# Kernel optimization log

Hardware: AMD Instinct MI355X
Metric: run time of the kernel (lower is better)

The kernel has to match this reference:

```python
import jax, jax.numpy as jnp
import numpy as np

N = 50000   # nodes
E = 800000  # edges
IN = 128    # input feature dim
HID = 64    # hidden per head
HEADS = 2
P = 100000  # pos/neg pairs
SLOPE = 0.2 # DGL GATConv default negative_slope
EPS = 1e-5  # BatchNorm eps


def setup_inputs() -> dict:
    key = jax.random.key(0)
    ks = jax.random.split(key, 40)
    nrm = lambda k, s, sc=0.1: jax.random.normal(k, s, jnp.float32) * sc
    inp = {}
    inp['x'] = jax.random.normal(ks[0], (N, IN), jnp.float32)
    inp['edge_src'] = jax.random.randint(ks[1], (E,), 0, N)
    inp['edge_dst'] = jax.random.randint(ks[2], (E,), 0, N)
    inp['pos_src'] = jax.random.randint(ks[3], (P,), 0, N)
    inp['pos_dst'] = jax.random.randint(ks[4], (P,), 0, N)
    inp['neg_src'] = jax.random.randint(ks[5], (P,), 0, N)
    inp['neg_dst'] = jax.random.randint(ks[6], (P,), 0, N)
    # GATConv layer 0: in=IN, out=HID, heads=HEADS
    inp['W0'] = nrm(ks[7], (IN, HEADS * HID))
    inp['al0'] = nrm(ks[8], (HEADS, HID))
    inp['ar0'] = nrm(ks[9], (HEADS, HID))
    inp['b0'] = jnp.zeros((HEADS * HID,), jnp.float32)
    # GATConv layer 1: in=HEADS*HID, out=HID, heads=HEADS
    inp['W1'] = nrm(ks[10], (HEADS * HID, HEADS * HID))
    inp['al1'] = nrm(ks[11], (HEADS, HID))
    inp['ar1'] = nrm(ks[12], (HEADS, HID))
    inp['b1'] = jnp.zeros((HEADS * HID,), jnp.float32)
    # GATConv layer 2: in=HEADS*HID, out=HID, heads=1
    inp['W2'] = nrm(ks[13], (HEADS * HID, HID))
    inp['al2'] = nrm(ks[14], (1, HID))
    inp['ar2'] = nrm(ks[15], (1, HID))
    inp['b2'] = jnp.zeros((HID,), jnp.float32)
    # BatchNorm params
    inp['bn0_g'] = jnp.ones((HEADS * HID,), jnp.float32)
    inp['bn0_b'] = jnp.zeros((HEADS * HID,), jnp.float32)
    inp['bn1_g'] = jnp.ones((HEADS * HID,), jnp.float32)
    inp['bn1_b'] = jnp.zeros((HEADS * HID,), jnp.float32)
    # predictor MLP: HID->HID->HID->1
    inp['pW1'] = nrm(ks[16], (HID, HID))
    inp['pb1'] = jnp.zeros((HID,), jnp.float32)
    inp['pW2'] = nrm(ks[17], (HID, HID))
    inp['pb2'] = jnp.zeros((HID,), jnp.float32)
    inp['pW3'] = nrm(ks[18], (HID, 1))
    inp['pb3'] = jnp.zeros((1,), jnp.float32)
    return inp


def gat_conv(h, src, dst, W, al, ar, b, heads, fh):
    # DGL GATConv: fc -> per-node attn dots -> edge LeakyReLU -> dst-segment softmax -> scatter-add
    feat = (h @ W).reshape(-1, heads, fh)            # [N, H, F]
    el = (feat * al[None]).sum(-1)                   # [N, H]
    er = (feat * ar[None]).sum(-1)                   # [N, H]
    e = jax.nn.leaky_relu(el[src] + er[dst], SLOPE)  # [E, H]
    m = jax.ops.segment_max(e, dst, num_segments=N)  # per-dst max for stability
    ee = jnp.exp(e - m[dst])
    denom = jax.ops.segment_sum(ee, dst, num_segments=N)
    alpha = ee / jnp.maximum(denom[dst], 1e-9)       # [E, H]
    out = jax.ops.segment_sum(alpha[:, :, None] * feat[src], dst, num_segments=N)
    return (out + b.reshape(1, heads, fh)).reshape(-1, heads * fh)


def batch_norm(h, g, b):
    mu = h.mean(0)
    var = jnp.var(h, 0)  # biased, matches torch BN training normalization
    return g * (h - mu) * jax.lax.rsqrt(var + EPS) + b


def predict(h_src, h_dst, pW1, pb1, pW2, pb2, pW3, pb3):
    z = h_src * h_dst
    z = jax.nn.relu(z @ pW1 + pb1)
    z = jax.nn.relu(z @ pW2 + pb2)
    return z @ pW3 + pb3


def reference(x, edge_src, edge_dst, pos_src, pos_dst, neg_src, neg_dst,
              W0, al0, ar0, b0, W1, al1, ar1, b1, W2, al2, ar2, b2,
              bn0_g, bn0_b, bn1_g, bn1_b, pW1, pb1, pW2, pb2, pW3, pb3):
    h = gat_conv(x, edge_src, edge_dst, W0, al0, ar0, b0, HEADS, HID)
    h = jax.nn.relu(batch_norm(h, bn0_g, bn0_b))  # dropout = identity (eval)
    h = gat_conv(h, edge_src, edge_dst, W1, al1, ar1, b1, HEADS, HID)
    h = jax.nn.relu(batch_norm(h, bn1_g, bn1_b))
    h = gat_conv(h, edge_src, edge_dst, W2, al2, ar2, b2, 1, HID)  # [N, HID]
    h_pos = predict(h[pos_src], h[pos_dst], pW1, pb1, pW2, pb2, pW3, pb3)
    h_neg = predict(h[neg_src], h[neg_dst], pW1, pb1, pW2, pb2, pW3, pb3)
    return (h_pos, h_neg)
```

## Files before the change

### kernel.cpp

```cpp
#include <hip/hip_runtime.h>
#include <hip/hip_fp16.h>
#include <cstdint>
#include <cstddef>

#define N_NODES 50000
#define N_EDGES 800000

typedef _Float16 f16x8 __attribute__((ext_vector_type(8)));
typedef float f32x4 __attribute__((ext_vector_type(4)));

__global__ void f32_to_f16(const float* __restrict__ in, __half* __restrict__ outp, int n4)
{
    int i = blockIdx.x * blockDim.x + threadIdx.x;
    int stride = gridDim.x * blockDim.x;
    for (; i < n4; i += stride) {
        float4 v = *reinterpret_cast<const float4*>(in + (size_t)i * 4);
        __half2 a = __floats2half2_rn(v.x, v.y);
        __half2 b = __floats2half2_rn(v.z, v.w);
        uint2 pk;
        pk.x = *reinterpret_cast<unsigned*>(&a);
        pk.y = *reinterpret_cast<unsigned*>(&b);
        *reinterpret_cast<uint2*>(outp + (size_t)i * 4) = pk;
    }
}

__global__ void prep_wt(const float* __restrict__ W0, const float* __restrict__ W1,
                        const float* __restrict__ W2, __half* __restrict__ t0,
                        __half* __restrict__ t1, __half* __restrict__ t2)
{
    int b = blockIdx.x >> 7;
    int k = blockIdx.x & 127;
    int c = threadIdx.x;
    const float* W = (b == 0) ? W0 : (b == 1) ? W1 : W2;
    __half* T = (b == 0) ? t0 : (b == 1) ? t1 : t2;
    int Cb = (b == 2) ? 64 : 128;
    if (c < Cb) T[(size_t)c * 128 + k] = __float2half(W[(size_t)k * Cb + c]);
}

template <int C, int H>
__launch_bounds__(256, 3)
__global__ void gemm_mfma(const __half* __restrict__ Ah, const __half* __restrict__ Wt,
                          const float* __restrict__ al, const float* __restrict__ ar,
                          __half* __restrict__ feat, float* __restrict__ el,
                          float* __restrict__ er, int n)
{
    constexpr int K = 128;
    constexpr int AS = 136;
    constexpr int CT = C / 16;
    __shared__ __half As[64 * AS];
    __shared__ __half Ws[C * AS];

    const int tid = threadIdx.x;
    const int brow = blockIdx.x * 64;

    for (int idx = tid; idx < 64 * 16; idx += 256) {
        int r = idx >> 4, u = idx & 15;
        int gr = brow + r;
        f16x8 v = {0, 0, 0, 0, 0, 0, 0, 0};
        if (gr < n) v = *reinterpret_cast<const f16x8*>(Ah + (size_t)gr * K + u * 8);
        *reinterpret_cast<f16x8*>(&As[r * AS + u * 8]) = v;
    }
    for (int idx = tid; idx < C * 16; idx += 256) {
        int c = idx >> 4, u = idx & 15;
        *reinterpret_cast<f16x8*>(&Ws[c * AS + u * 8]) =
            *reinterpret_cast<const f16x8*>(Wt + (size_t)c * K + u * 8);
    }
    __syncthreads();

    const int w = tid >> 6;
    const int l = tid & 63;
    const int l15 = l & 15;
    const int kg = l >> 4;

    f32x4 acc[CT];
    #pragma unroll
    for (int ct = 0; ct < CT; ++ct) acc[ct] = (f32x4){0.f, 0.f, 0.f, 0.f};

    #pragma unroll
    for (int kt = 0; kt < 4; ++kt) {
        f16x8 a = *reinterpret_cast<const f16x8*>(&As[(w * 16 + l15) * AS + kt * 32 + kg * 8]);
        #pragma unroll
        for (int ct = 0; ct < CT; ++ct) {
            f16x8 b = *reinterpret_cast<const f16x8*>(&Ws[(ct * 16 + l15) * AS + kt * 32 + kg * 8]);
            acc[ct] = __builtin_amdgcn_mfma_f32_16x16x32_f16(a, b, acc[ct], 0, 0, 0);
        }
    }

    const int row0 = w * 16 + kg * 4;
    float pel[4][H], per_[4][H];
    #pragma unroll
    for (int j = 0; j < 4; ++j)
        #pragma unroll
        for (int h = 0; h < H; ++h) { pel[j][h] = 0.f; per_[j][h] = 0.f; }

    #pragma unroll
    for (int ct = 0; ct < CT; ++ct) {
        int col = ct * 16 + l15;
        int head = (H == 2) ? (col >> 6) : 0;
        int lc = col & 63;
        float av = al[head * 64 + lc];
        float rv = ar[head * 64 + lc];
        #pragma unroll
        for (int j = 0; j < 4; ++j) {
            float fv = acc[ct][j];
            int gr = brow + row0 + j;
            if (gr < n) feat[(size_t)gr * C + col] = __float2half(fv);
            pel[j][head] += fv * av;
            per_[j][head] += fv * rv;
        }
    }
    #pragma unroll
    for (int off = 1; off < 16; off <<= 1) {
        #pragma unroll
        for (int j = 0; j < 4; ++j)
            #pragma unroll
            for (int h = 0; h < H; ++h) {
                pel[j][h] += __shfl_xor(pel[j][h], off, 64);
                per_[j][h] += __shfl_xor(per_[j][h], off, 64);
            }
    }
    if (l15 == 0) {
        #pragma unroll
        for (int j = 0; j < 4; ++j) {
            int gr = brow + row0 + j;
            if (gr < n) {
                if constexpr (H == 2) {
                    float2 e0 = make_float2(pel[j][0], pel[j][1]);
                    float2 e1 = make_float2(per_[j][0], per_[j][1]);
                    *reinterpret_cast<float2*>(el + (size_t)gr * 2) = e0;
                    *reinterpret_cast<float2*>(er + (size_t)gr * 2) = e1;
                } else {
                    el[gr] = pel[j][0];
                    er[gr] = per_[j][0];
                }
            }
        }
    }
}

__global__ void hist_dst(const int* __restrict__ dst, int* __restrict__ cnt, int E)
{
    int e = blockIdx.x * blockDim.x + threadIdx.x;
    if (e < E) atomicAdd(&cnt[dst[e]], 1);
}

__global__ void scan_block_sums(const int* __restrict__ cnt, int* __restrict__ bsum, int n)
{
    __shared__ int sh[256];
    int i = blockIdx.x * 256 + threadIdx.x;
    sh[threadIdx.x] = (i < n) ? cnt[i] : 0;
    __syncthreads();
    for (int off = 128; off; off >>= 1) {
        if (threadIdx.x < off) sh[threadIdx.x] += sh[threadIdx.x + off];
        __syncthreads();
    }
    if (threadIdx.x == 0) bsum[blockIdx.x] = sh[0];
}

__global__ void scan_bsum(int* __restrict__ bsum, int nb)
{
    __shared__ int sh[256];
    int t = threadIdx.x;
    sh[t] = (t < nb) ? bsum[t] : 0;
    __syncthreads();
    for (int off = 1; off < 256; off <<= 1) {
        int u = (t >= off) ? sh[t - off] : 0;
        __syncthreads();
        sh[t] += u;
        __syncthreads();
    }
    if (t < nb) bsum[t] = t ? sh[t - 1] : 0;
}

__global__ void scan_final(const int* __restrict__ cnt, const int* __restrict__ bsum,
                           int* __restrict__ rs, int* __restrict__ cursor, int n)
{
    __shared__ int sh[256];
    int t = threadIdx.x;
    int i = blockIdx.x * 256 + t;
    int v = (i < n) ? cnt[i] : 0;
    sh[t] = v;
    __syncthreads();
    for (int off = 1; off < 256; off <<= 1) {
        int u = (t >= off) ? sh[t - off] : 0;
        __syncthreads();
        sh[t] += u;
        __syncthreads();
    }
    int excl = sh[t] - v + bsum[blockIdx.x];
    if (i < n) { rs[i] = excl; cursor[i] = excl; }
    if (i == n - 1) rs[n] = excl + v;
}

__global__ void scatter_csr(const int* __restrict__ src, const int* __restrict__ dst,
                            int* __restrict__ cursor, int* __restrict__ csr, int E)
{
    int e = blockIdx.x * blockDim.x + threadIdx.x;
    if (e < E) {
        int d = dst[e];
        int pos = atomicAdd(&cursor[d], 1);
        csr[pos] = src[e];
    }
}

template <int C, int H>
__launch_bounds__(256)
__global__ void gat_agg(const int* __restrict__ rs, const int* __restrict__ csr,
                        const float* __restrict__ el, const float* __restrict__ er,
                        const __half* __restrict__ feat, const float* __restrict__ bias,
                        float* __restrict__ outp, int n)
{
    int node = blockIdx.x * 4 + (threadIdx.x >> 6);
    if (node >= n) return;
    int lane = threadIdx.x & 63;
    int start = rs[node], end = rs[node + 1];

    if constexpr (H == 2) {
        float2 e2 = *reinterpret_cast<const float2*>(er + (size_t)node * 2);
        float m0 = -INFINITY, m1 = -INFINITY;
        for (int j = start + lane; j < end; j += 64) {
            int s = csr[j];
            float2 l2 = *reinterpret_cast<const float2*>(el + (size_t)s * 2);
            float v0 = l2.x + e2.x; v0 = v0 >= 0.f ? v0 : 0.2f * v0;
            float v1 = l2.y + e2.y; v1 = v1 >= 0.f ? v1 : 0.2f * v1;
            m0 = fmaxf(m0, v0); m1 = fmaxf(m1, v1);
        }
        #pragma unroll
        for (int off = 32; off; off >>= 1) {
            m0 = fmaxf(m0, __shfl_xor(m0, off, 64));
            m1 = fmaxf(m1, __shfl_xor(m1, off, 64));
        }
        const int slot = lane >> 4;
        const int cl = lane & 15;
        const int h = cl >> 3;
        const float mh = h ? m1 : m0;
        const float erh = h ? e2.y : e2.x;
        float ssum = 0.f;
        float acc[8];
        #pragma unroll
        for (int u = 0; u < 8; ++u) acc[u] = 0.f;
        for (int j = start + slot; j < end; j += 4) {
            int s = csr[j];
            float v = el[(size_t)s * 2 + h] + erh;
            v = v >= 0.f ? v : 0.2f * v;
            float p = __expf(v - mh);
            ssum += p;
            float4 raw = *reinterpret_cast<const float4*>(feat + (size_t)s * C + cl * 8);
            const __half2* hp = reinterpret_cast<const __half2*>(&raw);
            #pragma unroll
            for (int u = 0; u < 4; ++u) {
                float2 f2 = __half22float2(hp[u]);
                acc[2 * u]     = fmaf(p, f2.x, acc[2 * u]);
                acc[2 * u + 1] = fmaf(p, f2.y, acc[2 * u + 1]);
            }
        }
        #pragma unroll
        for (int off = 16; off <= 32; off <<= 1) {
            ssum += __shfl_xor(ssum, off, 64);
            #pragma unroll
            for (int u = 0; u < 8; ++u) acc[u] += __shfl_xor(acc[u], off, 64);
        }
        if (slot == 0) {
            float r = 1.f / fmaxf(ssum, 1e-9f);
            float4 o0 = make_float4(acc[0] * r, acc[1] * r, acc[2] * r, acc[3] * r);
            float4 o1 = make_float4(acc[4] * r, acc[5] * r, acc[6] * r, acc[7] * r);
            *reinterpret_cast<float4*>(outp + (size_t)node * C + cl * 8) = o0;
            *reinterpret_cast<float4*>(outp + (size_t)node * C + cl * 8 + 4) = o1;
        }
    } else {
        float er0 = er[node];
        float m0 = -INFINITY;
        for (int j = start + lane; j < end; j += 64) {
            int s = csr[j];
            float v = el[s] + er0;
            v = v >= 0.f ? v : 0.2f * v;
            m0 = fmaxf(m0, v);
        }
        #pragma unroll
        for (int off = 32; off; off >>= 1)
            m0 = fmaxf(m0, __shfl_xor(m0, off, 64));
        const int slot = lane >> 3;
        const int cl = lane & 7;
        float ssum = 0.f;
        float acc[8];
        #pragma unroll
        for (int u = 0; u < 8; ++u) acc[u] = 0.f;
        for (int j = start + slot; j < end; j += 8) {
            int s = csr[j];
            float v = el[s] + er0;
            v = v >= 0.f ? v : 0.2f * v;
            float p = __expf(v - m0);
            ssum += p;
            float4 raw = *reinterpret_cast<const float4*>(feat + (size_t)s * C + cl * 8);
            const __half2* hp = reinterpret_cast<const __half2*>(&raw);
            #pragma unroll
            for (int u = 0; u < 4; ++u) {
                float2 f2 = __half22float2(hp[u]);
                acc[2 * u]     = fmaf(p, f2.x, acc[2 * u]);
                acc[2 * u + 1] = fmaf(p, f2.y, acc[2 * u + 1]);
            }
        }
        #pragma unroll
        for (int off = 8; off <= 32; off <<= 1) {
            ssum += __shfl_xor(ssum, off, 64);
            #pragma unroll
            for (int u = 0; u < 8; ++u) acc[u] += __shfl_xor(acc[u], off, 64);
        }
        if (slot == 0) {
            float r = 1.f / fmaxf(ssum, 1e-9f);
            float4 o0, o1;
            o0.x = acc[0] * r + bias[cl * 8 + 0];
            o0.y = acc[1] * r + bias[cl * 8 + 1];
            o0.z = acc[2] * r + bias[cl * 8 + 2];
            o0.w = acc[3] * r + bias[cl * 8 + 3];
            o1.x = acc[4] * r + bias[cl * 8 + 4];
            o1.y = acc[5] * r + bias[cl * 8 + 5];
            o1.z = acc[6] * r + bias[cl * 8 + 6];
            o1.w = acc[7] * r + bias[cl * 8 + 7];
            *reinterpret_cast<float4*>(outp + (size_t)node * C + cl * 8) = o0;
            *reinterpret_cast<float4*>(outp + (size_t)node * C + cl * 8 + 4) = o1;
        }
    }
}

__global__ void bn_stats(const float* __restrict__ h, float* __restrict__ sums, int n)
{
    __shared__ float s1[256], s2[256];
    int c = threadIdx.x & 127, half = threadIdx.x >> 7;
    float ls = 0.f, lq = 0.f;
    for (int r = blockIdx.x * 2 + half; r < n; r += gridDim.x * 2) {
        float v = h[(size_t)r * 128 + c];
        ls += v; lq += v * v;
    }
    s1[threadIdx.x] = ls; s2[threadIdx.x] = lq;
    __syncthreads();
    if (threadIdx.x < 128) {
        atomicAdd(&sums[c], s1[threadIdx.x] + s1[threadIdx.x + 128]);
        atomicAdd(&sums[128 + c], s2[threadIdx.x] + s2[threadIdx.x + 128]);
    }
}

__global__ void bn_apply(const float* __restrict__ in, __half* __restrict__ outp,
                         const float* __restrict__ sums,
                         const float* __restrict__ g, const float* __restrict__ b,
                         long long npairs)
{
    long long i = (long long)blockIdx.x * blockDim.x + threadIdx.x;
    if (i >= npairs) return;
    int c0 = (int)((i * 2) & 127);
    const float invN = 1.f / (float)N_NODES;
    float2 v = *reinterpret_cast<const float2*>(in + i * 2);
    float mean0 = sums[c0] * invN, mean1 = sums[c0 + 1] * invN;
    float var0 = sums[128 + c0] * invN - mean0 * mean0;
    float var1 = sums[128 + c0 + 1] * invN - mean1 * mean1;
    float o0 = fmaxf((v.x - mean0) * rsqrtf(var0 + 1e-5f) * g[c0] + b[c0], 0.f);
    float o1 = fmaxf((v.y - mean1) * rsqrtf(var1 + 1e-5f) * g[c0 + 1] + b[c0 + 1], 0.f);
    *reinterpret_cast<__half2*>(outp + i * 2) = __floats2half2_rn(o0, o1);
}

__launch_bounds__(256, 3)
__global__ void predictor(const float* __restrict__ h,
                          const int* __restrict__ ps, const int* __restrict__ pd,
                          const int* __restrict__ ns, const int* __restrict__ nd,
                          const float* __restrict__ W1, const float* __restrict__ b1,
                          const float* __restrict__ W2, const float* __restrict__ b2,
                          const float* __restrict__ W3, const float* __restrict__ b3,
                          float* __restrict__ out, int P)
{
    __shared__ float w1[64 * 64];
    __shared__ float w2[64 * 64];
    __shared__ float zt[64 * 68];
    const int tid = threadIdx.x;

    for (int i = tid; i < 1024; i += 256) {
        *reinterpret_cast<float4*>(&w1[i * 4]) = *reinterpret_cast<const float4*>(W1 + i * 4);
        *reinterpret_cast<float4*>(&w2[i * 4]) = *reinterpret_cast<const float4*>(W2 + i * 4);
    }

    {
        int l = tid & 63, w = tid >> 6;
        int gp = blockIdx.x * 64 + l;
        int s, d;
        if (gp < P) { s = ps[gp]; d = pd[gp]; }
        else        { s = ns[gp - P]; d = nd[gp - P]; }
        const float4* hs = reinterpret_cast<const float4*>(h + (size_t)s * 64 + w * 16);
        const float4* hd = reinterpret_cast<const float4*>(h + (size_t)d * 64 + w * 16);
        #pragma unroll
        for (int j = 0; j < 4; ++j) {
            float4 a = hs[j], b = hd[j];
            int c0 = w * 16 + j * 4;
            zt[(c0 + 0) * 68 + l] = a.x * b.x;
            zt[(c0 + 1) * 68 + l] = a.y * b.y;
            zt[(c0 + 2) * 68 + l] = a.z * b.z;
            zt[(c0 + 3) * 68 + l] = a.w * b.w;
        }
    }
    __syncthreads();

    const int pb = tid >> 4;
    const int cb = tid & 15;
    const int p0 = pb * 4, c0 = cb * 4;
    float4 vb1 = *reinterpret_cast<const float4*>(b1 + c0);
    float4 vb2 = *reinterpret_cast<const float4*>(b2 + c0);
    float4 vw3 = *reinterpret_cast<const float4*>(W3 + c0);
    const float b3v = b3[0];

    float acc[4][4];

    #pragma unroll
    for (int i = 0; i < 4; ++i)
        #pragma unroll
        for (int j = 0; j < 4; ++j) acc[i][j] = 0.f;

    #pragma unroll 4
    for (int k = 0; k < 64; ++k) {
        float4 zv = *reinterpret_cast<const float4*>(&zt[k * 68 + p0]);
        float4 wv = *reinterpret_cast<const float4*>(&w1[k * 64 + c0]);
        float zz[4] = {zv.x, zv.y, zv.z, zv.w};
        float ww[4] = {wv.x, wv.y, wv.z, wv.w};
        #pragma unroll
        for (int i = 0; i < 4; ++i)
            #pragma unroll
            for (int j = 0; j < 4; ++j)
                acc[i][j] = fmaf(zz[i], ww[j], acc[i][j]);
    }
    __syncthreads();
    {
        float bb[4] = {vb1.x, vb1.y, vb1.z, vb1.w};
        #pragma unroll
        for (int j = 0; j < 4; ++j) {
            float4 st = make_float4(fmaxf(acc[0][j] + bb[j], 0.f),
                                    fmaxf(acc[1][j] + bb[j], 0.f),
                                    fmaxf(acc[2][j] + bb[j], 0.f),
                                    fmaxf(acc[3][j] + bb[j], 0.f));
            *reinterpret_cast<float4*>(&zt[(c0 + j) * 68 + p0]) = st;
        }
    }
    __syncthreads();

    #pragma unroll
    for (int i = 0; i < 4; ++i)
        #pragma unroll
        for (int j = 0; j < 4; ++j) acc[i][j] = 0.f;

    #pragma unroll 4
    for (int k = 0; k < 64; ++k) {
        float4 zv = *reinterpret_cast<const float4*>(&zt[k * 68 + p0]);
        float4 wv = *reinterpret_cast<const float4*>(&w2[k * 64 + c0]);
        float zz[4] = {zv.x, zv.y, zv.z, zv.w};
        float ww[4] = {wv.x, wv.y, wv.z, wv.w};
        #pragma unroll
        for (int i = 0; i < 4; ++i)
            #pragma unroll
            for (int j = 0; j < 4; ++j)
                acc[i][j] = fmaf(zz[i], ww[j], acc[i][j]);
    }

    float part[4];
    {
        float bb[4] = {vb2.x, vb2.y, vb2.z, vb2.w};
        float w3v[4] = {vw3.x, vw3.y, vw3.z, vw3.w};
        #pragma unroll
        for (int i = 0; i < 4; ++i) {
            float su = 0.f;
            #pragma unroll
            for (int j = 0; j < 4; ++j)
                su += fmaxf(acc[i][j] + bb[j], 0.f) * w3v[j];
            part[i] = su;
        }
    }
    #pragma unroll
    for (int off = 1; off < 16; off <<= 1) {
        #pragma unroll
        for (int i = 0; i < 4; ++i)
            part[i] += __shfl_xor(part[i], off, 16);
    }
    if (cb == 0) {
        int gp0 = blockIdx.x * 64 + p0;
        #pragma unroll
        for (int i = 0; i < 4; ++i)
            out[gp0 + i] = part[i] + b3v;
    }
}

extern "C" void kernel_launch(void* const* d_in, const int* in_sizes, int n_in,
                              void* d_out, int out_size, void* d_ws, size_t ws_size,
                              hipStream_t stream)
{
    const float* x    = (const float*)d_in[0];
    const int* es     = (const int*)d_in[1];
    const int* ed     = (const int*)d_in[2];
    const int* ps     = (const int*)d_in[3];
    const int* pdst   = (const int*)d_in[4];
    const int* ns     = (const int*)d_in[5];
    const int* nd     = (const int*)d_in[6];
    const float* W0   = (const float*)d_in[7];
    const float* al0  = (const float*)d_in[8];
    const float* ar0  = (const float*)d_in[9];
    const float* W1   = (const float*)d_in[11];
    const float* al1  = (const float*)d_in[12];
    const float* ar1  = (const float*)d_in[13];
    const float* W2   = (const float*)d_in[15];
    const float* al2  = (const float*)d_in[16];
    const float* ar2  = (const float*)d_in[17];
    const float* b2   = (const float*)d_in[18];
    const float* bn0g = (const float*)d_in[19];
    const float* bn0b = (const float*)d_in[20];
    const float* bn1g = (const float*)d_in[21];
    const float* bn1b = (const float*)d_in[22];
    const float* pW1  = (const float*)d_in[23];
    const float* pb1  = (const float*)d_in[24];
    const float* pW2  = (const float*)d_in[25];
    const float* pb2  = (const float*)d_in[26];
    const float* pW3  = (const float*)d_in[27];
    const float* pb3  = (const float*)d_in[28];
    float* out = (float*)d_out;

    float* ws = (float*)d_ws;
    size_t off = 0;
    auto alloc = [&](size_t nelem) {
        float* p = ws + off;
        off += (nelem + 63) & ~(size_t)63;
        return p;
    };
    __half* featb = (__half*)alloc((size_t)N_NODES * 64);
    __half* xh    = (__half*)alloc((size_t)N_NODES * 64);
    float* hb    = alloc((size_t)N_NODES * 128);
    __half* wt0  = (__half*)alloc(128 * 64);
    __half* wt1  = (__half*)alloc(128 * 64);
    __half* wt2  = (__half*)alloc(64 * 64);
    float* el    = alloc((size_t)N_NODES * 2);
    float* er    = alloc((size_t)N_NODES * 2);
    float* bns   = alloc(256);
    int* cnt     = (int*)alloc(N_NODES);
    int* rs      = (int*)alloc(N_NODES + 1);
    int* cursor  = (int*)alloc(N_NODES);
    int* bsum    = (int*)alloc(256);
    int* csr     = (int*)alloc(N_EDGES);

    dim3 blk(256);
    const int gemmGrid = (N_NODES + 63) / 64;
    const int edgeGrid = (N_EDGES + 255) / 256;
    const int nodeBlocks = (N_NODES + 255) / 256;
    const int aggGrid = (N_NODES + 3) / 4;
    const long long bnPairs = (long long)N_NODES * 64;

    hipMemsetAsync(cnt, 0, (size_t)N_NODES * sizeof(int), stream);
    hist_dst<<<edgeGrid, blk, 0, stream>>>(ed, cnt, N_EDGES);
    scan_block_sums<<<nodeBlocks, blk, 0, stream>>>(cnt, bsum, N_NODES);
    scan_bsum<<<1, blk, 0, stream>>>(bsum, nodeBlocks);
    scan_final<<<nodeBlocks, blk, 0, stream>>>(cnt, bsum, rs, cursor, N_NODES);
    scatter_csr<<<edgeGrid, blk, 0, stream>>>(es, ed, cursor, csr, N_EDGES);
    f32_to_f16<<<2048, blk, 0, stream>>>(x, xh, N_NODES * 32);
    prep_wt<<<384, dim3(128), 0, stream>>>(W0, W1, W2, wt0, wt1, wt2);

    gemm_mfma<128, 2><<<gemmGrid, blk, 0, stream>>>(xh, wt0, al0, ar0, featb, el, er, N_NODES);
    gat_agg<128, 2><<<aggGrid, blk, 0, stream>>>(rs, csr, el, er, featb, nullptr, hb, N_NODES);
    hipMemsetAsync(bns, 0, 256 * sizeof(float), stream);
    bn_stats<<<256, blk, 0, stream>>>(hb, bns, N_NODES);
    bn_apply<<<(int)((bnPairs + 255) / 256), blk, 0, stream>>>(hb, xh, bns, bn0g, bn0b, bnPairs);

    gemm_mfma<128, 2><<<gemmGrid, blk, 0, stream>>>(xh, wt1, al1, ar1, featb, el, er, N_NODES);
    gat_agg<128, 2><<<aggGrid, blk, 0, stream>>>(rs, csr, el, er, featb, nullptr, hb, N_NODES);
    hipMemsetAsync(bns, 0, 256 * sizeof(float), stream);
    bn_stats<<<256, blk, 0, stream>>>(hb, bns, N_NODES);
    bn_apply<<<(int)((bnPairs + 255) / 256), blk, 0, stream>>>(hb, xh, bns, bn1g, bn1b, bnPairs);

    gemm_mfma<64, 1><<<gemmGrid, blk, 0, stream>>>(xh, wt2, al2, ar2, featb, el, er, N_NODES);
    gat_agg<64, 1><<<aggGrid, blk, 0, stream>>>(rs, csr, el, er, featb, b2, hb, N_NODES);

    predictor<<<3125, blk, 0, stream>>>(hb, ps, pdst, ns, nd,
                                        pW1, pb1, pW2, pb2, pW3, pb3, out, 100000);
}
```

Baseline: 502.7 us.

## Run predictor MLP on fp16 MFMA with half-precision gathered embeddings

```diff
diff --git a/kernel.cpp b/kernel.cpp
--- a/kernel.cpp
+++ b/kernel.cpp
@@ -35,6 +35,17 @@
     __half* T = (b == 0) ? t0 : (b == 1) ? t1 : t2;
     int Cb = (b == 2) ? 64 : 128;
     if (c < Cb) T[(size_t)c * 128 + k] = __float2half(W[(size_t)k * Cb + c]);
+}
+
+__global__ void prep_pwt(const float* __restrict__ W1, const float* __restrict__ W2,
+                         __half* __restrict__ t1, __half* __restrict__ t2)
+{
+    int b = blockIdx.x >> 6;
+    int k = blockIdx.x & 63;
+    int c = threadIdx.x;
+    const float* W = b ? W2 : W1;
+    __half* T = b ? t2 : t1;
+    T[(size_t)c * 64 + k] = __float2half(W[(size_t)k * 64 + c]);
 }
 
 template <int C, int H>
@@ -358,128 +369,108 @@
     *reinterpret_cast<__half2*>(outp + i * 2) = __floats2half2_rn(o0, o1);
 }
 
-__launch_bounds__(256, 3)
-__global__ void predictor(const float* __restrict__ h,
+__launch_bounds__(256, 5)
+__global__ void predictor(const __half* __restrict__ h16,
                           const int* __restrict__ ps, const int* __restrict__ pd,
                           const int* __restrict__ ns, const int* __restrict__ nd,
-                          const float* __restrict__ W1, const float* __restrict__ b1,
-                          const float* __restrict__ W2, const float* __restrict__ b2,
+                          const __half* __restrict__ W1t, const float* __restrict__ b1,
+                          const __half* __restrict__ W2t, const float* __restrict__ b2,
                           const float* __restrict__ W3, const float* __restrict__ b3,
                           float* __restrict__ out, int P)
 {
-    __shared__ float w1[64 * 64];
-    __shared__ float w2[64 * 64];
-    __shared__ float zt[64 * 68];
+    constexpr int AS = 72;
+    __shared__ __half zt[64 * AS];
+    __shared__ __half w1s[64 * AS];
+    __shared__ __half w2s[64 * AS];
     const int tid = threadIdx.x;
 
-    for (int i = tid; i < 1024; i += 256) {
-        *reinterpret_cast<float4*>(&w1[i * 4]) = *reinterpret_cast<const float4*>(W1 + i * 4);
-        *reinterpret_cast<float4*>(&w2[i * 4]) = *reinterpret_cast<const float4*>(W2 + i * 4);
+    for (int idx = tid; idx < 512; idx += 256) {
+        int c = idx >> 3, u = idx & 7;
+        *reinterpret_cast<f16x8*>(&w1s[c * AS + u * 8]) =
+            *reinterpret_cast<const f16x8*>(W1t + (size_t)c * 64 + u * 8);
+        *reinterpret_cast<f16x8*>(&w2s[c * AS + u * 8]) =
+            *reinterpret_cast<const f16x8*>(W2t + (size_t)c * 64 + u * 8);
     }
 
     {
-        int l = tid & 63, w = tid >> 6;
-        int gp = blockIdx.x * 64 + l;
+        int p = tid >> 2, q = tid & 3;
+        int gp = blockIdx.x * 64 + p;
         int s, d;
         if (gp < P) { s = ps[gp]; d = pd[gp]; }
         else        { s = ns[gp - P]; d = nd[gp - P]; }
-        const float4* hs = reinterpret_cast<const float4*>(h + (size_t)s * 64 + w * 16);
-        const float4* hd = reinterpret_cast<const float4*>(h + (size_t)d * 64 + w * 16);
-        #pragma unroll
-        for (int j = 0; j < 4; ++j) {
-            float4 a = hs[j], b = hd[j];
-            int c0 = w * 16 + j * 4;
-            zt[(c0 + 0) * 68 + l] = a.x * b.x;
-            zt[(c0 + 1) * 68 + l] = a.y * b.y;
-            zt[(c0 + 2) * 68 + l] = a.z * b.z;
-            zt[(c0 + 3) * 68 + l] = a.w * b.w;
-        }
-    }
-    __syncthreads();
-
-    const int pb = tid >> 4;
-    const int cb = tid & 15;
-    const int p0 = pb * 4, c0 = cb * 4;
-    float4 vb1 = *reinterpret_cast<const float4*>(b1 + c0);
-    float4 vb2 = *reinterpret_cast<const float4*>(b2 + c0);
-    float4 vw3 = *reinterpret_cast<const float4*>(W3 + c0);
-    const float b3v = b3[0];
-
-    float acc[4][4];
-
-    #pragma unroll
-    for (int i = 0; i < 4; ++i)
-        #pragma unroll
-        for (int j = 0; j < 4; ++j) acc[i][j] = 0.f;
-
-    #pragma unroll 4
-    for (int k = 0; k < 64; ++k) {
-        float4 zv = *reinterpret_cast<const float4*>(&zt[k * 68 + p0]);
-        float4 wv = *reinterpret_cast<const float4*>(&w1[k * 64 + c0]);
-        float zz[4] = {zv.x, zv.y, zv.z, zv.w};
-        float ww[4] = {wv.x, wv.y, wv.z, wv.w};
-        #pragma unroll
-        for (int i = 0; i < 4; ++i)
+        const f16x8* hs = reinterpret_cast<const f16x8*>(h16 + (size_t)s * 64 + q * 16);
+        const f16x8* hd = reinterpret_cast<const f16x8*>(h16 + (size_t)d * 64 + q * 16);
+        #pragma unroll
+        for (int u = 0; u < 2; ++u) {
+            f16x8 z = hs[u] * hd[u];
+            *reinterpret_cast<f16x8*>(&zt[p * AS + q * 16 + u * 8]) = z;
+        }
+    }
+    __syncthreads();
+
+    const int w = tid >> 6;
+    const int l = tid & 63;
+    const int l15 = l & 15;
+    const int kg = l >> 4;
+    const int myrow = (w * 16 + l15) * AS;
+
+    f32x4 acc[4];
+    {
+        f16x8 a0 = *reinterpret_cast<const f16x8*>(&zt[myrow + kg * 8]);
+        f16x8 a1 = *reinterpret_cast<const f16x8*>(&zt[myrow + 32 + kg * 8]);
+        #pragma unroll
+        for (int nt = 0; nt < 4; ++nt) {
+            f16x8 b0 = *reinterpret_cast<const f16x8*>(&w1s[(nt * 16 + l15) * AS + kg * 8]);
+            f16x8 b1v = *reinterpret_cast<const f16x8*>(&w1s[(nt * 16 + l15) * AS + 32 + kg * 8]);
+            acc[nt] = __builtin_amdgcn_mfma_f32_16x16x32_f16(a0, b0, (f32x4){0.f, 0.f, 0.f, 0.f}, 0, 0, 0);
+            acc[nt] = __builtin_amdgcn_mfma_f32_16x16x32_f16(a1, b1v, acc[nt], 0, 0, 0);
+        }
+    }
+    {
+        #pragma unroll
+        for (int nt = 0; nt < 4; ++nt) {
+            float bb = b1[nt * 16 + l15];
             #pragma unroll
-            for (int j = 0; j < 4; ++j)
-                acc[i][j] = fmaf(zz[i], ww[j], acc[i][j]);
-    }
-    __syncthreads();
+            for (int j = 0; j < 4; ++j) {
+                float v = fmaxf(acc[nt][j] + bb, 0.f);
+                zt[(w * 16 + kg * 4 + j) * AS + nt * 16 + l15] = __float2half(v);
+            }
+        }
+    }
+    __syncthreads();
+
     {
-        float bb[4] = {vb1.x, vb1.y, vb1.z, vb1.w};
-        #pragma unroll
-        for (int j = 0; j < 4; ++j) {
-            float4 st = make_float4(fmaxf(acc[0][j] + bb[j], 0.f),
-                                    fmaxf(acc[1][j] + bb[j], 0.f),
-                                    fmaxf(acc[2][j] + bb[j], 0.f),
-                                    fmaxf(acc[3][j] + bb[j], 0.f));
-            *reinterpret_cast<float4*>(&zt[(c0 + j) * 68 + p0]) = st;
-        }
-    }
-    __syncthreads();
-
-    #pragma unroll
-    for (int i = 0; i < 4; ++i)
-        #pragma unroll
-        for (int j = 0; j < 4; ++j) acc[i][j] = 0.f;
-
-    #pragma unroll 4
-    for (int k = 0; k < 64; ++k) {
-        float4 zv = *reinterpret_cast<const float4*>(&zt[k * 68 + p0]);
-        float4 wv = *reinterpret_cast<const float4*>(&w2[k * 64 + c0]);
-        float zz[4] = {zv.x, zv.y, zv.z, zv.w};
-        float ww[4] = {wv.x, wv.y, wv.z, wv.w};
-        #pragma unroll
-        for (int i = 0; i < 4; ++i)
-            #pragma unroll
-            for (int j = 0; j < 4; ++j)
-                acc[i][j] = fmaf(zz[i], ww[j], acc[i][j]);
-    }
-
-    float part[4];
-    {
-        float bb[4] = {vb2.x, vb2.y, vb2.z, vb2.w};
-        float w3v[4] = {vw3.x, vw3.y, vw3.z, vw3.w};
-        #pragma unroll
-        for (int i = 0; i < 4; ++i) {
-            float su = 0.f;
-            #pragma unroll
-            for (int j = 0; j < 4; ++j)
-                su += fmaxf(acc[i][j] + bb[j], 0.f) * w3v[j];
-            part[i] = su;
-        }
+        f16x8 a0 = *reinterpret_cast<const f16x8*>(&zt[myrow + kg * 8]);
+        f16x8 a1 = *reinterpret_cast<const f16x8*>(&zt[myrow + 32 + kg * 8]);
+        #pragma unroll
+        for (int nt = 0; nt < 4; ++nt) {
+            f16x8 b0 = *reinterpret_cast<const f16x8*>(&w2s[(nt * 16 + l15) * AS + kg * 8]);
+            f16x8 b1v = *reinterpret_cast<const f16x8*>(&w2s[(nt * 16 + l15) * AS + 32 + kg * 8]);
+            acc[nt] = __builtin_amdgcn_mfma_f32_16x16x32_f16(a0, b0, (f32x4){0.f, 0.f, 0.f, 0.f}, 0, 0, 0);
+            acc[nt] = __builtin_amdgcn_mfma_f32_16x16x32_f16(a1, b1v, acc[nt], 0, 0, 0);
+        }
+    }
+    float part[4] = {0.f, 0.f, 0.f, 0.f};
+    #pragma unroll
+    for (int nt = 0; nt < 4; ++nt) {
+        float bb = b2[nt * 16 + l15];
+        float wv = W3[nt * 16 + l15];
+        #pragma unroll
+        for (int j = 0; j < 4; ++j)
+            part[j] += fmaxf(acc[nt][j] + bb, 0.f) * wv;
     }
     #pragma unroll
     for (int off = 1; off < 16; off <<= 1) {
         #pragma unroll
-        for (int i = 0; i < 4; ++i)
-            part[i] += __shfl_xor(part[i], off, 16);
-    }
-    if (cb == 0) {
-        int gp0 = blockIdx.x * 64 + p0;
-        #pragma unroll
-        for (int i = 0; i < 4; ++i)
-            out[gp0 + i] = part[i] + b3v;
+        for (int j = 0; j < 4; ++j)
+            part[j] += __shfl_xor(part[j], off, 16);
+    }
+    if (l15 == 0) {
+        const float b3v = b3[0];
+        int gp0 = blockIdx.x * 64 + w * 16 + kg * 4;
+        #pragma unroll
+        for (int j = 0; j < 4; ++j)
+            out[gp0 + j] = part[j] + b3v;
     }
 }
 
@@ -529,6 +520,8 @@
     __half* wt0  = (__half*)alloc(128 * 64);
     __half* wt1  = (__half*)alloc(128 * 64);
     __half* wt2  = (__half*)alloc(64 * 64);
+    __half* pwt1 = (__half*)alloc(64 * 32);
+    __half* pwt2 = (__half*)alloc(64 * 32);
     float* el    = alloc((size_t)N_NODES * 2);
     float* er    = alloc((size_t)N_NODES * 2);
     float* bns   = alloc(256);
@@ -553,6 +546,7 @@
     scatter_csr<<<edgeGrid, blk, 0, stream>>>(es, ed, cursor, csr, N_EDGES);
     f32_to_f16<<<2048, blk, 0, stream>>>(x, xh, N_NODES * 32);
     prep_wt<<<384, dim3(128), 0, stream>>>(W0, W1, W2, wt0, wt1, wt2);
+    prep_pwt<<<128, dim3(64), 0, stream>>>(pW1, pW2, pwt1, pwt2);
 
     gemm_mfma<128, 2><<<gemmGrid, blk, 0, stream>>>(xh, wt0, al0, ar0, featb, el, er, N_NODES);
     gat_agg<128, 2><<<aggGrid, blk, 0, stream>>>(rs, csr, el, er, featb, nullptr, hb, N_NODES);
@@ -569,6 +563,7 @@
     gemm_mfma<64, 1><<<gemmGrid, blk, 0, stream>>>(xh, wt2, al2, ar2, featb, el, er, N_NODES);
     gat_agg<64, 1><<<aggGrid, blk, 0, stream>>>(rs, csr, el, er, featb, b2, hb, N_NODES);
 
-    predictor<<<3125, blk, 0, stream>>>(hb, ps, pdst, ns, nd,
-                                        pW1, pb1, pW2, pb2, pW3, pb3, out, 100000);
-}
+    f32_to_f16<<<2048, blk, 0, stream>>>(hb, xh, N_NODES * 16);
+    predictor<<<3125, blk, 0, stream>>>(xh, ps, pdst, ns, nd,
+                                        pwt1, pb1, pwt2, pb2, pW3, pb3, out, 100000);
+}
```

Result: faster. 467.6 us (-7.0%).
